# Performance work log

Measured on AMD Instinct MI355X. Metric: run time of the kernel, lower is better.

## Reference

```python
import jax, jax.numpy as jnp
import numpy as np

N, D, NUM_CLASSES = 8192, 512, 64


def setup_inputs() -> dict:
    key = jax.random.key(0)
    k1, k2 = jax.random.split(key)
    representations = jax.random.normal(k1, (N, D), dtype=jnp.float32)
    targets = jax.random.randint(k2, (N,), 0, NUM_CLASSES, dtype=jnp.int64)
    return {"representations": representations, "targets": targets}


def reference(representations, targets):
    # MSE branch of Consis_Reg:
    # S[i, j] = sum_d (A[i, d] - A[j, d])^2   (pairwise squared euclidean dist)
    # L_hat[i, j] = 1 if targets[j] == targets[i]
    # diag(L_hat @ S)[i] = sum_j L_hat[i, j] * S[j, i] = sum_{j: same label} S[i, j]
    # loss = sum_i diag_i / count_i
    A = representations
    sq = jnp.sum(A * A, axis=1)                      # [N]
    # ||a-b||^2 = ||a||^2 + ||b||^2 - 2 a.b  (GEMM form of the broadcast MSE sum)
    S = sq[:, None] + sq[None, :] - 2.0 * (A @ A.T)  # [N, N]
    mask = (targets[:, None] == targets[None, :]).astype(S.dtype)  # [N, N]
    per_row = jnp.sum(mask * S, axis=-1) / jnp.sum(mask, axis=-1)  # [N]
    return jnp.sum(per_row)
```

## Files before the change

### kernel.cpp

```cpp
#include <hip/hip_runtime.h>


#define N_ROWS 8192
#define DIM 512
#define NCLS 64
#define NWIN 16
#define WINROWS (N_ROWS / NWIN)
#define CAP 64

__device__ __forceinline__ float block_reduce_256(float v, float* sm) {
    #pragma unroll
    for (int off = 32; off > 0; off >>= 1)
        v += __shfl_down(v, off, 64);
    const int wave = threadIdx.x >> 6;
    const int lane = threadIdx.x & 63;
    if (lane == 0) sm[wave] = v;
    __syncthreads();
    v = (threadIdx.x < 4) ? sm[threadIdx.x] : 0.0f;
    if (wave == 0) {
        v += __shfl_down(v, 2, 64);
        v += __shfl_down(v, 1, 64);
    }
    __syncthreads();
    return v;
}

__global__ __launch_bounds__(256) void consis_accum(const float* __restrict__ A,
                                                    const int* __restrict__ tgt,
                                                    float* __restrict__ mpart,
                                                    float2* __restrict__ spart,
                                                    float* __restrict__ out) {
    __shared__ int lrows[CAP];
    __shared__ int lcnt;
    __shared__ float sred[4];

    const int c   = (int)(blockIdx.x >> 4);
    const int win = (int)(blockIdx.x & 15);

    if (threadIdx.x == 0) lcnt = 0;
    __syncthreads();

    const int base = win * WINROWS;
    #pragma unroll
    for (int k = 0; k < WINROWS / 256; ++k) {
        const int i = base + k * 256 + (int)threadIdx.x;
        if (tgt[i] == c) {
            const int p = atomicAdd(&lcnt, 1);
            if (p < CAP) lrows[p] = i;
        }
    }
    __syncthreads();

    const int total = lcnt;
    int n = total > CAP ? CAP : total;

    const int col = (int)threadIdx.x * 2;
    float mx = 0.0f, my = 0.0f, sacc = 0.0f;
    #pragma unroll 4
    for (int k = 0; k < n; ++k) {
        const int r = lrows[k];
        const float2 v = *(const float2*)(A + (size_t)r * DIM + col);
        mx += v.x;
        my += v.y;
        sacc += v.x * v.x + v.y * v.y;
    }

    float2 st; st.x = mx; st.y = my;
    *(float2*)(mpart + (size_t)blockIdx.x * DIM + col) = st;

    const float s = block_reduce_256(sacc, sred);
    if (threadIdx.x == 0) {
        spart[blockIdx.x] = make_float2(s, (float)total);
        if (blockIdx.x == 0) out[0] = 0.0f;
    }
}

__global__ __launch_bounds__(256) void consis_finish(const float* __restrict__ mpart,
                                                     const float2* __restrict__ spart,
                                                     float* __restrict__ out) {
    __shared__ float sred[4];
    __shared__ float nsh;
    const int c = (int)blockIdx.x;

    float2 sp = make_float2(0.0f, 0.0f);
    if (threadIdx.x < NWIN) sp = spart[c * NWIN + (int)threadIdx.x];

    const float ncf = block_reduce_256(sp.y, sred);
    if (threadIdx.x == 0) nsh = ncf;
    __syncthreads();
    const float n = nsh;
    const float inv = (n > 0.0f) ? (2.0f / n) : 0.0f;

    const int col = (int)threadIdx.x * 2;
    const float* mp = mpart + (size_t)c * NWIN * DIM + col;
    float mx = 0.0f, my = 0.0f;
    #pragma unroll
    for (int w = 0; w < NWIN; ++w) {
        const float2 v = *(const float2*)(mp + (size_t)w * DIM);
        mx += v.x;
        my += v.y;
    }

    const float contrib = 2.0f * sp.x - inv * (mx * mx + my * my);
    const float tot = block_reduce_256(contrib, sred);
    if (threadIdx.x == 0) atomicAdd(out, tot);
}

extern "C" void kernel_launch(void* const* d_in, const int* in_sizes, int n_in,
                              void* d_out, int out_size, void* d_ws, size_t ws_size,
                              hipStream_t stream) {
    const float* A   = (const float*)d_in[0];
    const int*   tgt = (const int*)d_in[1];
    float* out   = (float*)d_out;
    float* mpart = (float*)d_ws;
    float2* spart = (float2*)((char*)d_ws +
                    (size_t)NCLS * NWIN * DIM * sizeof(float));

    consis_accum<<<NCLS * NWIN, 256, 0, stream>>>(A, tgt, mpart, spart, out);
    consis_finish<<<NCLS, 256, 0, stream>>>(mpart, spart, out);
}
```

Measured before the change: 69.14 us.

## Fuse accumulate and finish kernels into one cooperative kernel with grid sync

Merges the per-window accumulation kernel and the per-class finishing kernel into a single cooperative launch. A grid-wide sync separates the two phases, which removes the second kernel launch and its dependency gap. The finishing reduction is also restructured to reduce three values in one pass instead of two sequential block reductions. In exchange it depends on the cooperative launch succeeding with 1024 co-resident blocks, adds grid-barrier cost, and keeps the two-kernel path as a fallback if the launch fails.

```diff
diff --git a/kernel.cpp b/kernel.cpp
--- a/kernel.cpp
+++ b/kernel.cpp
@@ -1,4 +1,7 @@
 #include <hip/hip_runtime.h>
+#include <hip/hip_cooperative_groups.h>
+
+namespace cg = cooperative_groups;
 
 
 #define N_ROWS 8192
@@ -7,6 +10,7 @@
 #define NWIN 16
 #define WINROWS (N_ROWS / NWIN)
 #define CAP 64
+#define NBLK (NCLS * NWIN)
 
 __device__ __forceinline__ float block_reduce_256(float v, float* sm) {
     #pragma unroll
@@ -16,28 +20,42 @@
     const int lane = threadIdx.x & 63;
     if (lane == 0) sm[wave] = v;
     __syncthreads();
-    v = (threadIdx.x < 4) ? sm[threadIdx.x] : 0.0f;
-    if (wave == 0) {
-        v += __shfl_down(v, 2, 64);
-        v += __shfl_down(v, 1, 64);
-    }
+    float r = 0.0f;
+    if (threadIdx.x == 0) r = sm[0] + sm[1] + sm[2] + sm[3];
     __syncthreads();
-    return v;
+    return r;
 }
 
-__global__ __launch_bounds__(256) void consis_accum(const float* __restrict__ A,
-                                                    const int* __restrict__ tgt,
-                                                    float* __restrict__ mpart,
-                                                    float2* __restrict__ spart,
-                                                    float* __restrict__ out) {
-    __shared__ int lrows[CAP];
-    __shared__ int lcnt;
-    __shared__ float sred[4];
+__device__ __forceinline__ void block_reduce3(float& a, float& b, float& c,
+                                              float* sm ) {
+    #pragma unroll
+    for (int off = 32; off > 0; off >>= 1) {
+        a += __shfl_down(a, off, 64);
+        b += __shfl_down(b, off, 64);
+        c += __shfl_down(c, off, 64);
+    }
+    const int wave = threadIdx.x >> 6;
+    const int lane = threadIdx.x & 63;
+    if (lane == 0) { sm[wave] = a; sm[4 + wave] = b; sm[8 + wave] = c; }
+    __syncthreads();
+    if (threadIdx.x == 0) {
+        a = sm[0] + sm[1] + sm[2] + sm[3];
+        b = sm[4] + sm[5] + sm[6] + sm[7];
+        c = sm[8] + sm[9] + sm[10] + sm[11];
+    }
+}
 
-    const int c   = (int)(blockIdx.x >> 4);
-    const int win = (int)(blockIdx.x & 15);
+__device__ __forceinline__ void accum_phase(const float* __restrict__ A,
+                                            const int* __restrict__ tgt,
+                                            float* __restrict__ mpart,
+                                            float2* __restrict__ spart,
+                                            float* __restrict__ out,
+                                            int bid, float* sred,
+                                            int* lrows, int* lcnt) {
+    const int c   = bid >> 4;
+    const int win = bid & 15;
 
-    if (threadIdx.x == 0) lcnt = 0;
+    if (threadIdx.x == 0) *lcnt = 0;
     __syncthreads();
 
     const int base = win * WINROWS;
@@ -45,13 +63,13 @@
     for (int k = 0; k < WINROWS / 256; ++k) {
         const int i = base + k * 256 + (int)threadIdx.x;
         if (tgt[i] == c) {
-            const int p = atomicAdd(&lcnt, 1);
+            const int p = atomicAdd(lcnt, 1);
             if (p < CAP) lrows[p] = i;
         }
     }
     __syncthreads();
 
-    const int total = lcnt;
+    const int total = *lcnt;
     int n = total > CAP ? CAP : total;
 
     const int col = (int)threadIdx.x * 2;
@@ -66,30 +84,21 @@
     }
 
     float2 st; st.x = mx; st.y = my;
-    *(float2*)(mpart + (size_t)blockIdx.x * DIM + col) = st;
+    *(float2*)(mpart + (size_t)bid * DIM + col) = st;
 
     const float s = block_reduce_256(sacc, sred);
     if (threadIdx.x == 0) {
-        spart[blockIdx.x] = make_float2(s, (float)total);
-        if (blockIdx.x == 0) out[0] = 0.0f;
+        spart[bid] = make_float2(s, (float)total);
+        if (bid == 0) out[0] = 0.0f;
     }
 }
 
-__global__ __launch_bounds__(256) void consis_finish(const float* __restrict__ mpart,
-                                                     const float2* __restrict__ spart,
-                                                     float* __restrict__ out) {
-    __shared__ float sred[4];
-    __shared__ float nsh;
-    const int c = (int)blockIdx.x;
-
+__device__ __forceinline__ void finish_phase(const float* __restrict__ mpart,
+                                             const float2* __restrict__ spart,
+                                             float* __restrict__ out,
+                                             int c, float* sred) {
     float2 sp = make_float2(0.0f, 0.0f);
     if (threadIdx.x < NWIN) sp = spart[c * NWIN + (int)threadIdx.x];
-
-    const float ncf = block_reduce_256(sp.y, sred);
-    if (threadIdx.x == 0) nsh = ncf;
-    __syncthreads();
-    const float n = nsh;
-    const float inv = (n > 0.0f) ? (2.0f / n) : 0.0f;
 
     const int col = (int)threadIdx.x * 2;
     const float* mp = mpart + (size_t)c * NWIN * DIM + col;
@@ -101,9 +110,49 @@
         my += v.y;
     }
 
-    const float contrib = 2.0f * sp.x - inv * (mx * mx + my * my);
-    const float tot = block_reduce_256(contrib, sred);
-    if (threadIdx.x == 0) atomicAdd(out, tot);
+    float a = sp.x;
+    float b = sp.y;
+    float msq = mx * mx + my * my;
+    block_reduce3(a, b, msq, sred);
+    if (threadIdx.x == 0 && b > 0.0f)
+        atomicAdd(out, 2.0f * a - 2.0f * msq / b);
+}
+
+__global__ __launch_bounds__(256) void consis_fused(const float* __restrict__ A,
+                                                    const int* __restrict__ tgt,
+                                                    float* __restrict__ mpart,
+                                                    float2* __restrict__ spart,
+                                                    float* __restrict__ out) {
+    __shared__ int lrows[CAP];
+    __shared__ int lcnt;
+    __shared__ float sred[12];
+
+    const int bid = (int)blockIdx.x;
+    accum_phase(A, tgt, mpart, spart, out, bid, sred, lrows, &lcnt);
+
+    __threadfence();
+    cg::this_grid().sync();
+
+    if (bid < NCLS)
+        finish_phase(mpart, spart, out, bid, sred);
+}
+
+__global__ __launch_bounds__(256) void consis_accum(const float* __restrict__ A,
+                                                    const int* __restrict__ tgt,
+                                                    float* __restrict__ mpart,
+                                                    float2* __restrict__ spart,
+                                                    float* __restrict__ out) {
+    __shared__ int lrows[CAP];
+    __shared__ int lcnt;
+    __shared__ float sred[12];
+    accum_phase(A, tgt, mpart, spart, out, (int)blockIdx.x, sred, lrows, &lcnt);
+}
+
+__global__ __launch_bounds__(256) void consis_finish(const float* __restrict__ mpart,
+                                                     const float2* __restrict__ spart,
+                                                     float* __restrict__ out) {
+    __shared__ float sred[12];
+    finish_phase(mpart, spart, out, (int)blockIdx.x, sred);
 }
 
 extern "C" void kernel_launch(void* const* d_in, const int* in_sizes, int n_in,
@@ -116,6 +165,12 @@
     float2* spart = (float2*)((char*)d_ws +
                     (size_t)NCLS * NWIN * DIM * sizeof(float));
 
-    consis_accum<<<NCLS * NWIN, 256, 0, stream>>>(A, tgt, mpart, spart, out);
-    consis_finish<<<NCLS, 256, 0, stream>>>(mpart, spart, out);
+    void* args[] = {(void*)&A, (void*)&tgt, (void*)&mpart, (void*)&spart, (void*)&out};
+    hipError_t err = hipLaunchCooperativeKernel((const void*)consis_fused,
+                                                dim3(NBLK), dim3(256),
+                                                args, 0, stream);
+    if (err != hipSuccess) {
+        consis_accum<<<NBLK, 256, 0, stream>>>(A, tgt, mpart, spart, out);
+        consis_finish<<<NCLS, 256, 0, stream>>>(mpart, spart, out);
+    }
 }
```

Result: slower. 215.8 us (+212.1%).
